# Performance work log

Hardware: AMD Instinct MI355X
Metric: run time of the kernel (lower is better)

The kernel has to match this reference:

```python
import jax, jax.numpy as jnp
import numpy as np

V, D, N, K, T, S = 128000, 128, 4, 4, 16, 5
EPS = 1e-10


def setup_inputs() -> dict:
    key = jax.random.key(0)
    k = jax.random.split(key, 5)
    return {
        "E": jax.random.normal(k[0], (V, D), jnp.float32) * 0.02,
        "bases": jax.random.normal(k[1], (K, N, D, D), jnp.float32) * (1.5 / np.sqrt(D)),
        "tension": jax.random.normal(k[2], (K, N, N), jnp.float32) * 0.1,
        "temperature": jnp.ones((K,), jnp.float32),
        "target_sim": jnp.full((K,), -1.0 / (N - 1), jnp.float32),
        "step_size": jnp.full((K,), 0.1, jnp.float32),
        "gate_logit": jnp.full((K,), -2.0, jnp.float32),
        "decay_base": jnp.asarray(0.8, jnp.float32),
        "sensitivity": jnp.asarray(1.0, jnp.float32),
        "noise": jax.random.normal(k[3], (T, K, S, N, D), jnp.float32),
        "tokens": jax.random.randint(k[4], (T,), 0, V),
    }


def reference(E, bases, tension, temperature, target_sim, step_size, gate_logit,
              decay_base, sensitivity, noise, tokens):
    mask = 1.0 - jnp.eye(N, dtype=E.dtype)
    temp = jnp.clip(jnp.abs(temperature), 0.01, None)
    # gauge interaction weights per foam: softmax over bubbles, self-interaction masked
    interaction = jax.nn.softmax(-tension / temp[:, None, None], axis=-1) * mask  # [K,N,N]
    step = jnp.clip(jnp.abs(step_size), 0.001, 0.5)           # [K]
    gate = jax.nn.sigmoid(gate_logit)                          # [K] noise gate
    sens = jnp.abs(sensitivity)

    def equilibrate(state0, B, inter, tgt, stp, g, nz):
        # state0 [N,D]; B [N,D,D] per-bubble bases; nz [S,N,D] pre-drawn perturbations
        def body(state, eps):
            expr = jnp.einsum('nd,nkd->nk', state, B)          # state_i @ basis_i.T
            expr_n = expr / (jnp.linalg.norm(expr, axis=-1, keepdims=True) + EPS)
            cos = expr_n @ expr_n.T                            # [N,N] pairwise cos-sim
            fmag = (cos - tgt) * inter                         # [N,N] force magnitudes
            diff = expr[:, None, :] - expr[None, :, :]         # [N,N,D]
            diff_n = diff / (jnp.linalg.norm(diff, axis=-1, keepdims=True) + EPS)
            f_shared = (fmag[..., None] * diff_n).sum(axis=1)  # [N,D]
            f_local = jnp.einsum('nk,nkd->nd', f_shared, B)    # back to local gauge
            scale = jnp.linalg.norm(state, axis=-1).mean() + EPS
            return state + stp * f_local + g * eps * scale * 0.01, None
        state, _ = jax.lax.scan(body, state0, nz)
        return state

    def foam_step(x, memory, B, inter, tgt, stp, g, nz):
        # x [D]; memory [N,D]
        mem_mean = memory.mean(axis=0)
        mem_norm = jnp.linalg.norm(mem_mean) + EPS
        x_norm = jnp.linalg.norm(x) + EPS
        nov = 1.0 - (x * mem_mean).sum() / (x_norm * mem_norm)
        novelty = jnp.where(mem_norm > 1e-8, nov, 1.0)
        decay = jax.nn.sigmoid(decay_base - sens * novelty)
        xm = x + decay * mem_mean
        eq = equilibrate(jnp.broadcast_to(xm, (N, D)), B, inter, tgt, stp, g, nz)
        rho = (eq.T @ eq) / ((eq * eq).sum() + EPS)            # trace-normalized density
        mem_new = decay * memory + (1.0 - decay) * eq
        return rho, mem_new

    xs_tok = E[tokens]                                         # [T,D]

    def token_step(memories, inp):
        x, nz_t = inp
        rhos, memories = jax.vmap(foam_step, in_axes=(None, 0, 0, 0, 0, 0, 0, 0))(
            x, memories, bases, interaction, target_sim, step, gate, nz_t)
        rho_mix = rhos.mean(axis=0)                            # [D,D]
        eig = jnp.clip(jnp.linalg.eigvalsh(rho_mix), 1e-12, None)
        eig = eig / eig.sum()
        logits = ((E @ rho_mix) * E).sum(axis=-1)              # born rule [V]
        logp = jax.nn.log_softmax(logits)
        probs = jnp.exp(logp)
        S_rho = -(eig * jnp.clip(jnp.log(eig), -100.0, None)).sum()
        H_tok = -(probs * jnp.clip(logp, -100.0, None)).sum()
        return memories, (probs, S_rho, H_tok, H_tok - S_rho)

    mem0 = jnp.zeros((K, N, D), E.dtype)
    _, (probs, S_rho, H_tok, F_tok) = jax.lax.scan(token_step, mem0, (xs_tok, noise))
    return probs, S_rho, H_tok, F_tok
```

## Files before the change

### kernel.cpp

```cpp
#include <hip/hip_runtime.h>
#include <math.h>

#define V_ 128000
#define D_ 128
#define N_ 4
#define K_ 4
#define T_ 16
#define S_ 5
#define EPSF 1e-10f

#define WS_G      0
#define WS_BEPS   262144
#define WS_BX     917504
#define WS_EQBALL 954368
#define WS_INTER  977408
#define WS_WK     977472
#define WS_SRHO   977728
#define WS_LNZ    977744
#define WS_ZPART  977760
#define WS_HPART  1009760

typedef __attribute__((ext_vector_type(8))) short short8v;
typedef __attribute__((ext_vector_type(4))) float float4v;

__device__ __forceinline__ short bfb(float x) {
    unsigned u = __float_as_uint(x);
    u += 0x7fffu + ((u >> 16) & 1u);
    return (short)(u >> 16);
}

__device__ __forceinline__ void jpair(int x, int r, int& ox, bool& isp) {
    if (x == 15) { ox = r % 15; isp = true; return; }
    int s = x - r; s %= 15; if (s < 0) s += 15;
    if (s == 0) { ox = 15; isp = false; return; }
    int o = 2 * r - x; o %= 15; if (o < 0) o += 15;
    ox = o;
    isp = (s <= 7);
}

__device__ __forceinline__ void rotfast(float app, float aqq, float apq, float& c, float& s) {
    c = 1.f; s = 0.f;
    if (fabsf(apq) > 1e-20f) {
        float tau = (aqq - app) * 0.5f * __builtin_amdgcn_rcpf(apq);
        float sq1 = __builtin_amdgcn_sqrtf(1.f + tau * tau);
        float den = tau + ((tau >= 0.f) ? sq1 : -sq1);
        float tt = __builtin_amdgcn_rcpf(den);
        c = __builtin_amdgcn_rsqf(1.f + tt * tt);
        s = tt * c;
    }
}

__global__ __launch_bounds__(256)
void i2_prep(const float* __restrict__ bases, const float* __restrict__ E,
             const float* __restrict__ noise, const int* __restrict__ tokens,
             const float* __restrict__ tension, const float* __restrict__ temperature,
             float* __restrict__ ws)
{
    int tid = threadIdx.x;
    if (blockIdx.x == 64) {
        if (tid < 4) {
            int k = tid;
            float temp = fmaxf(fabsf(temperature[k]), 0.01f);
            for (int i = 0; i < 4; ++i) {
                float v[4]; float mx = -1e30f;
                for (int j = 0; j < 4; ++j) { v[j] = -tension[k*16 + i*4 + j] / temp; mx = fmaxf(mx, v[j]); }
                float se = 0.f;
                for (int j = 0; j < 4; ++j) { v[j] = expf(v[j] - mx); se += v[j]; }
                for (int j = 0; j < 4; ++j) ws[WS_INTER + k*16 + i*4 + j] = (i == j) ? 0.0f : v[j] / se;
            }
        }
        return;
    }
    int kn = blockIdx.x >> 2, q = blockIdx.x & 3;
    int k = kn >> 2, n = kn & 3;
    __shared__ __align__(16) float Blds[128 * 132];
    const float4* B4 = (const float4*)(bases + (size_t)kn * 16384);
    for (int idx = tid; idx < 4096; idx += 256) {
        int jrow = idx >> 5, c = idx & 31;
        float4 v = B4[jrow * 32 + c];
        *((float4*)&Blds[jrow * 132 + c * 4]) = v;
    }
    __syncthreads();
    int j1 = q * 32 + (tid >> 3);
    int l = tid & 7;
    float accg[16];
#pragma unroll
    for (int i = 0; i < 16; ++i) accg[i] = 0.f;
    for (int c = 0; c < 32; ++c) {
        float4 b1 = *((const float4*)&Blds[j1 * 132 + c * 4]);
#pragma unroll
        for (int i = 0; i < 16; ++i) {
            float4 b2 = *((const float4*)&Blds[(l + 8 * i) * 132 + c * 4]);
            accg[i] += b1.x * b2.x + b1.y * b2.y + b1.z * b2.z + b1.w * b2.w;
        }
    }
#pragma unroll
    for (int i = 0; i < 16; ++i) {
        int j2 = l + 8 * i;
        ws[WS_G + (((size_t)kn * 32 + (j2 >> 2)) * 128 + j1) * 4 + (j2 & 3)] = accg[i];
    }
    __shared__ __align__(16) float vecl[128];
    __shared__ float vred[2][128];
    int jv = tid & 127, ch = tid >> 7;
    for (int vi = q * 24; vi < q * 24 + 24; ++vi) {
        const float* src; int dstoff;
        if (vi < 16) {
            int tt = vi;
            src = E + (size_t)tokens[tt] * 128;
            dstoff = WS_BX + (tt * 4 + k) * 512 + n * 128;
        } else {
            int r2 = vi - 16; int tt = r2 / 5, s2 = r2 % 5;
            size_t off = (size_t)(((tt * 4 + k) * 5 + s2) * 4 + n) * 128;
            src = noise + off;
            dstoff = WS_BEPS + (int)off;
        }
        if (tid < 32) ((float4*)vecl)[tid] = ((const float4*)src)[tid];
        __syncthreads();
        float a2 = 0.f;
        for (int c = ch * 16; c < ch * 16 + 16; ++c) {
            float4 bv = *((const float4*)&Blds[jv * 132 + c * 4]);
            float4 xv = ((const float4*)vecl)[c];
            a2 += bv.x * xv.x + bv.y * xv.y + bv.z * xv.z + bv.w * xv.w;
        }
        vred[ch][jv] = a2;
        __syncthreads();
        if (tid < 128) ws[dstoff + tid] = vred[0][tid] + vred[1][tid];
        __syncthreads();
    }
}

__global__ __launch_bounds__(512, 2)
void kap_all(const float* __restrict__ E, const float* __restrict__ noise,
             const int* __restrict__ tokens, const float* __restrict__ bases,
             const float* __restrict__ target_sim, const float* __restrict__ step_size,
             const float* __restrict__ gate_logit, const float* __restrict__ decay_base,
             const float* __restrict__ sensitivity, float* __restrict__ ws)
{
    const int k = blockIdx.x;
    const int tid = threadIdx.x;
    const int w = tid >> 6;
    const int n = w & 3;
    const int h = w >> 2;
    const int lane = tid & 63;
    const int d0 = lane, d1 = lane + 64;
    const int dG = h * 64 + lane;
    const int kn = k * 4 + n;

    __shared__ float xl[128];
    __shared__ float mlL[128];
    __shared__ __align__(16) float aL[4][128];
    __shared__ float exL[4][128];
    __shared__ float bmmL[4][128];
    __shared__ float interL[16];
    __shared__ float diagP[4], sP[4];
    __shared__ float sq7[4][2];

    float4 gg[32];
    const float4* G4 = (const float4*)(ws + WS_G);
#pragma unroll
    for (int c = 0; c < 32; ++c) gg[c] = G4[((size_t)kn * 32 + c) * 128 + dG];

    if (tid < 16) interL[tid] = ws[WS_INTER + k * 16 + tid];
    if (tid < 128) mlL[tid] = 0.f;
    bmmL[n][dG] = 0.f;

    const float tgt = target_sim[k];
    const float stp = fminf(fmaxf(fabsf(step_size[k]), 0.001f), 0.5f);
    const float gate = 1.0f / (1.0f + expf(-gate_logit[k]));
    const float dbase = decay_base[0];
    const float sens = fabsf(sensitivity[0]);

    float xr = (tid < 128) ? E[(size_t)tokens[0] * 128 + tid] : 0.f;
    __syncthreads();
    float w_inter[4];
#pragma unroll
    for (int m = 0; m < 4; ++m) w_inter[m] = interL[n * 4 + m];

#pragma unroll 1
    for (int t = 0; t < T_; ++t) {
        if (tid < 128) xl[tid] = xr;
        __syncthreads();
        if (t + 1 < T_ && tid < 128) xr = E[(size_t)tokens[t + 1] * 128 + tid];

        float bep0[5], bep1[5], no0[5], no1[5];
#pragma unroll
        for (int s = 0; s < 5; ++s) {
            int nz = (((t * 4 + k) * 5 + s) * 4 + n) * 128;
            bep0[s] = ws[WS_BEPS + nz + d0]; bep1[s] = ws[WS_BEPS + nz + d1];
            no0[s] = noise[nz + d0];         no1[s] = noise[nz + d1];
        }
        float bx0 = ws[WS_BX + (t * 4 + k) * 512 + n * 128 + d0];
        float bx1 = ws[WS_BX + (t * 4 + k) * 512 + n * 128 + d1];

        float x0 = xl[d0], x1 = xl[d1], m0 = mlL[d0], m1 = mlL[d1];
        float vx = x0 * x0 + x1 * x1, vm = m0 * m0 + m1 * m1, vd = x0 * m0 + x1 * m1;
        for (int m = 32; m; m >>= 1) { vx += __shfl_xor(vx, m); vm += __shfl_xor(vm, m); vd += __shfl_xor(vd, m); }
        float xnorm = sqrtf(vx) + EPSF, mnorm = sqrtf(vm) + EPSF;
        float nov = 1.0f - vd / (xnorm * mnorm);
        float novelty = (mnorm > 1e-8f) ? nov : 1.0f;
        const float dec = 1.0f / (1.0f + expf(-(dbase - sens * novelty)));

        float bm0 = bmmL[n][d0], bm1 = bmmL[n][d1];
        float e00 = bx0 + dec * bm0, e01 = bx1 + dec * bm1;
        float u0 = x0 + dec * m0, u1 = x1 + dec * m1;
        float a0 = 0.f, a1 = 0.f, be0 = 0.f, be1 = 0.f;
        exL[n][dG] = (h == 0) ? e00 : e01;
        __syncthreads();

        for (int s = 0; s < 5; ++s) {
            float em0[4], em1[4];
#pragma unroll
            for (int m = 0; m < 4; ++m) { em0[m] = exL[m][d0]; em1[m] = exL[m][d1]; }
            float ex0 = em0[n], ex1 = em1[n];
            float r[5];
#pragma unroll
            for (int m = 0; m < 4; ++m) r[m] = ex0 * em0[m] + ex1 * em1[m];
            float t4 = u0 * u0 + u1 * u1;
            float t5 = (e00 + be0) * a0 + (e01 + be1) * a1;
            float t6 = a0 * (ex0 - e00 - be0) + a1 * (ex1 - e01 - be1);
            r[4] = t4 + 2.f * t5 + t6;
#pragma unroll
            for (int m2 = 32; m2; m2 >>= 1) {
#pragma unroll
                for (int q = 0; q < 5; ++q) r[q] += __shfl_xor(r[q], m2);
            }
            float sn = sqrtf(fmaxf(r[4], 0.f));
            if (lane == 0 && h == 0) { diagP[n] = r[n]; sP[n] = sn; }
            __syncthreads();
            float ssum = ((sP[0] + sP[1]) + sP[2]) + sP[3];
            float cn = gate * (0.25f * ssum + EPSF) * 0.01f;

            float Pnn = r[n];
            float enn = sqrtf(fmaxf(Pnn, 0.f)) + EPSF;
            float fsh0 = 0.f, fsh1 = 0.f;
#pragma unroll
            for (int m = 0; m < 4; ++m) {
                float Pmm = diagP[m];
                float Pnm = r[m];
                float enm = sqrtf(fmaxf(Pmm, 0.f)) + EPSF;
                float cosnm = Pnm / (enn * enm);
                float fm = (cosnm - tgt) * w_inter[m];
                float dnn = sqrtf(fmaxf(Pnn - 2.f * Pnm + Pmm, 0.f)) + EPSF;
                float wq = fm / dnn;
                fsh0 += wq * (ex0 - em0[m]);
                fsh1 += wq * (ex1 - em1[m]);
            }
            a0 += stp * fsh0; a1 += stp * fsh1;
            be0 += cn * bep0[s]; be1 += cn * bep1[s];
            u0 += cn * no0[s];   u1 += cn * no1[s];
            aL[n][d0] = a0; aL[n][d1] = a1;
            const float4* a4 = (const float4*)aL[n];
            float y = 0.f;
#pragma unroll
            for (int c = 0; c < 32; ++c) {
                float4 av = a4[c];
                y += gg[c].x * av.x + gg[c].y * av.y + gg[c].z * av.z + gg[c].w * av.w;
            }
            float exn = ((h == 0) ? e00 : e01) + y + ((h == 0) ? be0 : be1);
            exL[n][dG] = exn;
            __syncthreads();
        }

        {
            const float* Bp = bases + (size_t)kn * 16384;
            float acc = 0.f;
#pragma unroll 8
            for (int j = 0; j < 128; ++j) acc += aL[n][j] * Bp[(size_t)j * 128 + dG];
            float eq = ((h == 0) ? u0 : u1) + acc;
            ws[WS_BEPS + t * 10240 + k * 2560 + n * 128 + dG] = eq;
            unsigned short* eqb = (unsigned short*)(ws + WS_EQBALL);
            {
                int c2 = dG >> 5, lg = (dG >> 3) & 3, j8 = dG & 7;
                eqb[t * 2048 + (c2 * 64 + lg * 16 + kn) * 8 + j8] = (unsigned short)bfb(eq);
            }
            float sq = eq * eq;
            for (int m = 32; m; m >>= 1) sq += __shfl_xor(sq, m);
            if (lane == 0) sq7[n][h] = sq;
            exL[n][dG] = eq;
            __syncthreads();
            if (tid < 4) {
                float s4 = (sq7[0][0] + sq7[0][1]) + (sq7[1][0] + sq7[1][1])
                         + (sq7[2][0] + sq7[2][1]) + (sq7[3][0] + sq7[3][1]);
                ws[WS_WK + t * 16 + 4 * k + tid] = 1.0f / (4.0f * (s4 + EPSF));
            }
            if (n == 0) {
                float eqm = 0.25f * (exL[0][dG] + exL[1][dG] + exL[2][dG] + exL[3][dG]);
                mlL[dG] = dec * mlL[dG] + (1.f - dec) * eqm;
            }
            __syncthreads();
            const float4* Br = (const float4*)(bases + (size_t)kn * 16384 + (size_t)dG * 128);
            const float4* mm4 = (const float4*)mlL;
            float bacc = 0.f;
#pragma unroll 8
            for (int c = 0; c < 32; ++c) {
                float4 mv = mm4[c];
                float4 bv = Br[c];
                bacc += bv.x * mv.x + bv.y * mv.y + bv.z * mv.z + bv.w * mv.w;
            }
            bmmL[n][dG] = bacc;
        }
    }
}

__global__ __launch_bounds__(256, 2)
void mega(const float* __restrict__ E, float* __restrict__ ws, float* __restrict__ out)
{
    int b = blockIdx.x, tid = threadIdx.x;
    if (b < 16) {
        int tt = b;
        __shared__ float Gsh[256];
        __shared__ float Am[16 * 20];
        __shared__ float cR[16], sR[16];
        {
            int i = tid >> 4, j = tid & 15;
            const float4* ra = (const float4*)(ws + WS_BEPS + tt * 10240 + (i >> 2) * 2560 + (i & 3) * 128);
            const float4* rb = (const float4*)(ws + WS_BEPS + tt * 10240 + (j >> 2) * 2560 + (j & 3) * 128);
            float dp = 0.f;
#pragma unroll 8
            for (int c = 0; c < 32; ++c) {
                float4 a = ra[c], b2 = rb[c];
                dp += a.x * b2.x + a.y * b2.y + a.z * b2.z + a.w * b2.w;
            }
            Gsh[tid] = dp;
        }
        __syncthreads();
        if (tid >= 64) return;
        const float* G = Gsh;
        int i0 = tid >> 2, j40 = (tid & 3) * 4;
        float wv4[4];
#pragma unroll
        for (int kk = 0; kk < 4; ++kk) {
            float ss = G[(4*kk+0)*17] + G[(4*kk+1)*17] + G[(4*kk+2)*17] + G[(4*kk+3)*17];
            wv4[kk] = 1.0f / (4.0f * (ss + EPSF));
        }
#pragma unroll
        for (int m = 0; m < 4; ++m) {
            int jjv = j40 + m;
            Am[i0 * 20 + jjv] = sqrtf(wv4[i0 >> 2] * wv4[jjv >> 2]) * G[i0 * 16 + jjv];
        }
        for (int sw = 0; sw < 6; ++sw) {
            for (int r = 0; r < 15; ++r) {
                if (tid < 8) {
                    int p, q;
                    if (tid == 0) { p = 15; q = r % 15; }
                    else { p = (r + tid) % 15; q = (r - tid + 15) % 15; }
                    float c, s;
                    rotfast(Am[p * 20 + p], Am[q * 20 + q], Am[p * 20 + q], c, s);
                    cR[p] = c; sR[p] = -s;
                    cR[q] = c; sR[q] = s;
                }
                int oi; bool ip; jpair(i0, r, oi, ip);
                float ci = cR[i0], siS = sR[i0];
                float nv[4];
#pragma unroll
                for (int m = 0; m < 4; ++m) {
                    int jjv = j40 + m;
                    int oj; bool jp2; jpair(jjv, r, oj, jp2);
                    float cj = cR[jjv], sjS = sR[jjv];
                    float a00 = Am[i0 * 20 + jjv], a01 = Am[i0 * 20 + oj];
                    float a10 = Am[oi * 20 + jjv], a11 = Am[oi * 20 + oj];
                    nv[m] = ci*cj*a00 + ci*sjS*a01 + siS*cj*a10 + siS*sjS*a11;
                }
#pragma unroll
                for (int m = 0; m < 4; ++m) Am[i0 * 20 + j40 + m] = nv[m];
            }
        }
        if (tid == 0) {
            float tot = 112.0f * 1e-12f;
            float lc[16];
            for (int a2 = 0; a2 < 16; ++a2) { lc[a2] = fmaxf(Am[a2 * 20 + a2], 1e-12f); tot += lc[a2]; }
            float S = 0.f;
            for (int a2 = 0; a2 < 16; ++a2) { float pp = lc[a2] / tot; S -= pp * fmaxf(logf(pp), -100.f); }
            float p0 = 1e-12f / tot;
            S -= 112.f * p0 * fmaxf(logf(p0), -100.f);
            out[(size_t)T_ * V_ + tt] = S;
            ws[WS_SRHO + tt] = S;
        }
        return;
    }
    int b2 = b - 16;
    int pass = b2 / 500;
    int bb = b2 - pass * 500;
    int tok0 = pass * 8;
    int lane = tid & 63, wv = tid >> 6;
    const short8v* eqB = (const short8v*)(ws + WS_EQBALL);
    short8v bfr[8][4];
#pragma unroll
    for (int tk = 0; tk < 8; ++tk)
#pragma unroll
        for (int c2 = 0; c2 < 4; ++c2) bfr[tk][c2] = eqB[(tok0 + tk) * 256 + c2 * 64 + lane];
    float wk[8], zl[8];
#pragma unroll
    for (int tk = 0; tk < 8; ++tk) {
        wk[tk] = ws[WS_WK + (tok0 + tk) * 16 + (lane & 15)];
        zl[tk] = 0.f;
    }
    int tilebase = (bb * 4 + wv) * 64;
#pragma unroll
    for (int it = 0; it < 4; ++it) {
        int rowB = tilebase + it * 16;
        const float* Erow = E + (size_t)(rowB + (lane & 15)) * 128 + ((lane >> 4) * 8);
        float4v acc[8];
#pragma unroll
        for (int tk = 0; tk < 8; ++tk) acc[tk] = (float4v){0.f, 0.f, 0.f, 0.f};
#pragma unroll
        for (int c2 = 0; c2 < 4; ++c2) {
            float4 e0 = *((const float4*)(Erow + c2 * 32));
            float4 e1 = *((const float4*)(Erow + c2 * 32 + 4));
            short8v a;
            a[0] = bfb(e0.x); a[1] = bfb(e0.y); a[2] = bfb(e0.z); a[3] = bfb(e0.w);
            a[4] = bfb(e1.x); a[5] = bfb(e1.y); a[6] = bfb(e1.z); a[7] = bfb(e1.w);
#pragma unroll
            for (int tk = 0; tk < 8; ++tk)
                acc[tk] = __builtin_amdgcn_mfma_f32_16x16x32_bf16(a, bfr[tk][c2], acc[tk], 0, 0, 0);
        }
#pragma unroll
        for (int tk = 0; tk < 8; ++tk) {
            float l0 = wk[tk] * acc[tk][0] * acc[tk][0];
            float l1 = wk[tk] * acc[tk][1] * acc[tk][1];
            float l2 = wk[tk] * acc[tk][2] * acc[tk][2];
            float l3 = wk[tk] * acc[tk][3] * acc[tk][3];
#pragma unroll
            for (int m = 1; m <= 8; m <<= 1) {
                l0 += __shfl_xor(l0, m); l1 += __shfl_xor(l1, m);
                l2 += __shfl_xor(l2, m); l3 += __shfl_xor(l3, m);
            }
            if ((lane & 15) == 0) {
                float4 st; st.x = l0; st.y = l1; st.z = l2; st.w = l3;
                *((float4*)(out + (size_t)(tok0 + tk) * V_ + rowB + (lane >> 4) * 4)) = st;
                zl[tk] += __expf(l0) + __expf(l1) + __expf(l2) + __expf(l3);
            }
        }
    }
#pragma unroll
    for (int tk = 0; tk < 8; ++tk) {
        float z = zl[tk];
        z += __shfl_xor(z, 16); z += __shfl_xor(z, 32);
        if (lane == 0) ws[WS_ZPART + (tok0 + tk) * 2000 + bb * 4 + wv] = z;
    }
}

__global__ __launch_bounds__(256)
void zk(float* __restrict__ ws)
{
    int b = blockIdx.x, tid = threadIdx.x;
    double s = 0.0;
    for (int i = tid; i < 2000; i += 256) s += (double)ws[WS_ZPART + b * 2000 + i];
    for (int m = 32; m; m >>= 1) s += __shfl_xor(s, m);
    __shared__ double sr[4];
    if ((tid & 63) == 0) sr[tid >> 6] = s;
    __syncthreads();
    if (tid == 0) ws[WS_LNZ + b] = (float)log(sr[0] + sr[1] + sr[2] + sr[3]);
}

__global__ __launch_bounds__(256)
void fin1(float* __restrict__ ws, float* __restrict__ out)
{
    int b = blockIdx.x, tid = threadIdx.x;
    int tt = b / 125, blk = b - tt * 125;
    int v = blk * 1024 + tid * 4;
    float lnZ = ws[WS_LNZ + tt];
    float* po = out + (size_t)tt * V_ + v;
    float4 l4 = *((const float4*)po);
    float lp0 = l4.x - lnZ, lp1 = l4.y - lnZ, lp2 = l4.z - lnZ, lp3 = l4.w - lnZ;
    float p0 = __expf(lp0), p1 = __expf(lp1), p2 = __expf(lp2), p3 = __expf(lp3);
    float4 st; st.x = p0; st.y = p1; st.z = p2; st.w = p3;
    *((float4*)po) = st;
    float hp = p0 * fmaxf(lp0, -100.f) + p1 * fmaxf(lp1, -100.f)
             + p2 * fmaxf(lp2, -100.f) + p3 * fmaxf(lp3, -100.f);
    for (int m = 32; m; m >>= 1) hp += __shfl_xor(hp, m);
    __shared__ float hr[4];
    if ((tid & 63) == 0) hr[tid >> 6] = hp;
    __syncthreads();
    if (tid == 0) ws[WS_HPART + tt * 125 + blk] = hr[0] + hr[1] + hr[2] + hr[3];
}

__global__ __launch_bounds__(128)
void f2_final(float* __restrict__ ws, float* __restrict__ out)
{
    int t = blockIdx.x, tid = threadIdx.x;
    float s = (tid < 125) ? ws[WS_HPART + t * 125 + tid] : 0.f;
    for (int m = 32; m; m >>= 1) s += __shfl_xor(s, m);
    __shared__ float sr[2];
    if ((tid & 63) == 0) sr[tid >> 6] = s;
    __syncthreads();
    if (tid == 0) {
        float H = -(sr[0] + sr[1]);
        float S = ws[WS_SRHO + t];
        out[(size_t)T_ * V_ + T_ + t] = H;
        out[(size_t)T_ * V_ + 2 * T_ + t] = H - S;
    }
}

extern "C" void kernel_launch(void* const* d_in, const int* in_sizes, int n_in,
                              void* d_out, int out_size, void* d_ws, size_t ws_size,
                              hipStream_t stream)
{
    (void)in_sizes; (void)n_in; (void)out_size; (void)ws_size;
    const float* E           = (const float*)d_in[0];
    const float* bases       = (const float*)d_in[1];
    const float* tension     = (const float*)d_in[2];
    const float* temperature = (const float*)d_in[3];
    const float* target_sim  = (const float*)d_in[4];
    const float* step_size   = (const float*)d_in[5];
    const float* gate_logit  = (const float*)d_in[6];
    const float* decay_base  = (const float*)d_in[7];
    const float* sensitivity = (const float*)d_in[8];
    const float* noise       = (const float*)d_in[9];
    const int*   tokens      = (const int*)d_in[10];
    float* out = (float*)d_out;
    float* ws  = (float*)d_ws;

    i2_prep<<<65, 256, 0, stream>>>(bases, E, noise, tokens, tension, temperature, ws);
    kap_all<<<4, 512, 0, stream>>>(E, noise, tokens, bases, target_sim, step_size,
                                   gate_logit, decay_base, sensitivity, ws);
    mega<<<1016, 256, 0, stream>>>(E, ws, out);
    zk<<<16, 256, 0, stream>>>(ws);
    fin1<<<T_ * 125, 256, 0, stream>>>(ws, out);
    f2_final<<<T_, 128, 0, stream>>>(ws, out);
}
```

Before: 599.8 us.

## Restructure equilibration loop: double-buffer shared state, drop barrier, DPP reductions

Each wave now computes the pairwise dot products and diagonal norms itself from shared expression vectors, using DPP-based wavefront reductions. This removes one of the two block barriers per inner iteration. Expression vectors and the squared-norm partials are double-buffered, and the memory-basis product is kept in registers instead of shared memory. The G matrix is streamed from global memory each iteration rather than held in 128 registers, which lowers register pressure but adds repeated global or cache traffic. Dot products use several independent accumulators to shorten dependency chains.

```diff
diff --git a/kernel.cpp b/kernel.cpp
--- a/kernel.cpp
+++ b/kernel.cpp
@@ -27,6 +27,16 @@
     unsigned u = __float_as_uint(x);
     u += 0x7fffu + ((u >> 16) & 1u);
     return (short)(u >> 16);
+}
+
+__device__ __forceinline__ float wred64(float x) {
+    x += __int_as_float(__builtin_amdgcn_update_dpp(0, __float_as_int(x), 0xB1, 0xf, 0xf, true));
+    x += __int_as_float(__builtin_amdgcn_update_dpp(0, __float_as_int(x), 0x4E, 0xf, 0xf, true));
+    x += __int_as_float(__builtin_amdgcn_update_dpp(0, __float_as_int(x), 0x141, 0xf, 0xf, true));
+    x += __int_as_float(__builtin_amdgcn_update_dpp(0, __float_as_int(x), 0x140, 0xf, 0xf, true));
+    x += __shfl_xor(x, 16);
+    x += __shfl_xor(x, 32);
+    return x;
 }
 
 __device__ __forceinline__ void jpair(int x, int r, int& ox, bool& isp) {
@@ -149,28 +159,26 @@
     __shared__ float xl[128];
     __shared__ float mlL[128];
     __shared__ __align__(16) float aL[4][128];
-    __shared__ float exL[4][128];
-    __shared__ float bmmL[4][128];
+    __shared__ float exb[2][4][128];
     __shared__ float interL[16];
-    __shared__ float diagP[4], sP[4];
+    __shared__ float sPb[2][4][2];
     __shared__ float sq7[4][2];
 
-    float4 gg[32];
-    const float4* G4 = (const float4*)(ws + WS_G);
-#pragma unroll
-    for (int c = 0; c < 32; ++c) gg[c] = G4[((size_t)kn * 32 + c) * 128 + dG];
+    const float4* Gw = (const float4*)(ws + WS_G) + (size_t)kn * 4096 + dG;
+    const float*  Bcol = bases + (size_t)kn * 16384 + dG;
+    const float4* Br0 = (const float4*)(bases + (size_t)kn * 16384 + (size_t)d0 * 128);
+    const float4* Br1 = (const float4*)(bases + (size_t)kn * 16384 + (size_t)d1 * 128);
 
     if (tid < 16) interL[tid] = ws[WS_INTER + k * 16 + tid];
-    if (tid < 128) mlL[tid] = 0.f;
-    bmmL[n][dG] = 0.f;
+    if (tid < 128) { mlL[tid] = 0.f; xl[tid] = E[(size_t)tokens[0] * 128 + tid]; }
 
     const float tgt = target_sim[k];
     const float stp = fminf(fmaxf(fabsf(step_size[k]), 0.001f), 0.5f);
     const float gate = 1.0f / (1.0f + expf(-gate_logit[k]));
     const float dbase = decay_base[0];
     const float sens = fabsf(sensitivity[0]);
-
-    float xr = (tid < 128) ? E[(size_t)tokens[0] * 128 + tid] : 0.f;
+    float bm0 = 0.f, bm1 = 0.f;
+    float xr = 0.f;
     __syncthreads();
     float w_inter[4];
 #pragma unroll
@@ -178,10 +186,6 @@
 
 #pragma unroll 1
     for (int t = 0; t < T_; ++t) {
-        if (tid < 128) xl[tid] = xr;
-        __syncthreads();
-        if (t + 1 < T_ && tid < 128) xr = E[(size_t)tokens[t + 1] * 128 + tid];
-
         float bep0[5], bep1[5], no0[5], no1[5];
 #pragma unroll
         for (int s = 0; s < 5; ++s) {
@@ -191,51 +195,53 @@
         }
         float bx0 = ws[WS_BX + (t * 4 + k) * 512 + n * 128 + d0];
         float bx1 = ws[WS_BX + (t * 4 + k) * 512 + n * 128 + d1];
+        if (t + 1 < T_ && tid < 128) xr = E[(size_t)tokens[t + 1] * 128 + tid];
 
         float x0 = xl[d0], x1 = xl[d1], m0 = mlL[d0], m1 = mlL[d1];
-        float vx = x0 * x0 + x1 * x1, vm = m0 * m0 + m1 * m1, vd = x0 * m0 + x1 * m1;
-        for (int m = 32; m; m >>= 1) { vx += __shfl_xor(vx, m); vm += __shfl_xor(vm, m); vd += __shfl_xor(vd, m); }
+        float vx = wred64(x0 * x0 + x1 * x1);
+        float vm = wred64(m0 * m0 + m1 * m1);
+        float vd = wred64(x0 * m0 + x1 * m1);
         float xnorm = sqrtf(vx) + EPSF, mnorm = sqrtf(vm) + EPSF;
         float nov = 1.0f - vd / (xnorm * mnorm);
         float novelty = (mnorm > 1e-8f) ? nov : 1.0f;
         const float dec = 1.0f / (1.0f + expf(-(dbase - sens * novelty)));
 
-        float bm0 = bmmL[n][d0], bm1 = bmmL[n][d1];
         float e00 = bx0 + dec * bm0, e01 = bx1 + dec * bm1;
         float u0 = x0 + dec * m0, u1 = x1 + dec * m1;
         float a0 = 0.f, a1 = 0.f, be0 = 0.f, be1 = 0.f;
-        exL[n][dG] = (h == 0) ? e00 : e01;
+        {
+            float uh = (h == 0) ? u0 : u1;
+            float r4h = wred64(uh * uh);
+            if (lane == 0) sPb[0][n][h] = r4h;
+        }
+        exb[0][n][dG] = (h == 0) ? e00 : e01;
         __syncthreads();
 
+#pragma unroll
         for (int s = 0; s < 5; ++s) {
+            const int rb = s & 1, wb = rb ^ 1;
             float em0[4], em1[4];
 #pragma unroll
-            for (int m = 0; m < 4; ++m) { em0[m] = exL[m][d0]; em1[m] = exL[m][d1]; }
+            for (int m = 0; m < 4; ++m) { em0[m] = exb[rb][m][d0]; em1[m] = exb[rb][m][d1]; }
             float ex0 = em0[n], ex1 = em1[n];
-            float r[5];
-#pragma unroll
-            for (int m = 0; m < 4; ++m) r[m] = ex0 * em0[m] + ex1 * em1[m];
-            float t4 = u0 * u0 + u1 * u1;
-            float t5 = (e00 + be0) * a0 + (e01 + be1) * a1;
-            float t6 = a0 * (ex0 - e00 - be0) + a1 * (ex1 - e01 - be1);
-            r[4] = t4 + 2.f * t5 + t6;
-#pragma unroll
-            for (int m2 = 32; m2; m2 >>= 1) {
-#pragma unroll
-                for (int q = 0; q < 5; ++q) r[q] += __shfl_xor(r[q], m2);
-            }
-            float sn = sqrtf(fmaxf(r[4], 0.f));
-            if (lane == 0 && h == 0) { diagP[n] = r[n]; sP[n] = sn; }
-            __syncthreads();
-            float ssum = ((sP[0] + sP[1]) + sP[2]) + sP[3];
+            float ssum = sqrtf(fmaxf(sPb[rb][0][0] + sPb[rb][0][1], 0.f))
+                       + sqrtf(fmaxf(sPb[rb][1][0] + sPb[rb][1][1], 0.f))
+                       + sqrtf(fmaxf(sPb[rb][2][0] + sPb[rb][2][1], 0.f))
+                       + sqrtf(fmaxf(sPb[rb][3][0] + sPb[rb][3][1], 0.f));
             float cn = gate * (0.25f * ssum + EPSF) * 0.01f;
 
+            float r[4], dm[4];
+#pragma unroll
+            for (int m = 0; m < 4; ++m) {
+                r[m]  = wred64(ex0 * em0[m] + ex1 * em1[m]);
+                dm[m] = wred64(em0[m] * em0[m] + em1[m] * em1[m]);
+            }
             float Pnn = r[n];
             float enn = sqrtf(fmaxf(Pnn, 0.f)) + EPSF;
             float fsh0 = 0.f, fsh1 = 0.f;
 #pragma unroll
             for (int m = 0; m < 4; ++m) {
-                float Pmm = diagP[m];
+                float Pmm = dm[m];
                 float Pnm = r[m];
                 float enm = sqrtf(fmaxf(Pmm, 0.f)) + EPSF;
                 float cosnm = Pnm / (enn * enm);
@@ -250,33 +256,46 @@
             u0 += cn * no0[s];   u1 += cn * no1[s];
             aL[n][d0] = a0; aL[n][d1] = a1;
             const float4* a4 = (const float4*)aL[n];
-            float y = 0.f;
+            float ya = 0.f, yb = 0.f, yc = 0.f, yd = 0.f;
 #pragma unroll
             for (int c = 0; c < 32; ++c) {
+                float4 gv = Gw[(size_t)c * 128];
                 float4 av = a4[c];
-                y += gg[c].x * av.x + gg[c].y * av.y + gg[c].z * av.z + gg[c].w * av.w;
-            }
+                ya += gv.x * av.x; yb += gv.y * av.y;
+                yc += gv.z * av.z; yd += gv.w * av.w;
+            }
+            float y = (ya + yb) + (yc + yd);
             float exn = ((h == 0) ? e00 : e01) + y + ((h == 0) ? be0 : be1);
-            exL[n][dG] = exn;
+            exb[wb][n][dG] = exn;
+            if (s < 4) {
+                float uh = (h == 0) ? u0 : u1;
+                float ebh = (h == 0) ? (e00 + be0) : (e01 + be1);
+                float ah = (h == 0) ? a0 : a1;
+                float r4h = wred64(uh * uh + 2.f * (ebh * ah) + ah * y);
+                if (lane == 0) sPb[wb][n][h] = r4h;
+            }
             __syncthreads();
         }
 
         {
-            const float* Bp = bases + (size_t)kn * 16384;
-            float acc = 0.f;
-#pragma unroll 8
-            for (int j = 0; j < 128; ++j) acc += aL[n][j] * Bp[(size_t)j * 128 + dG];
-            float eq = ((h == 0) ? u0 : u1) + acc;
+            float eA = 0.f, eB = 0.f, eC = 0.f, eD = 0.f;
+#pragma unroll
+            for (int j = 0; j < 128; j += 4) {
+                eA += aL[n][j]     * Bcol[(size_t)j * 128];
+                eB += aL[n][j + 1] * Bcol[(size_t)(j + 1) * 128];
+                eC += aL[n][j + 2] * Bcol[(size_t)(j + 2) * 128];
+                eD += aL[n][j + 3] * Bcol[(size_t)(j + 3) * 128];
+            }
+            float eq = ((h == 0) ? u0 : u1) + ((eA + eB) + (eC + eD));
             ws[WS_BEPS + t * 10240 + k * 2560 + n * 128 + dG] = eq;
             unsigned short* eqb = (unsigned short*)(ws + WS_EQBALL);
             {
                 int c2 = dG >> 5, lg = (dG >> 3) & 3, j8 = dG & 7;
                 eqb[t * 2048 + (c2 * 64 + lg * 16 + kn) * 8 + j8] = (unsigned short)bfb(eq);
             }
-            float sq = eq * eq;
-            for (int m = 32; m; m >>= 1) sq += __shfl_xor(sq, m);
+            float sq = wred64(eq * eq);
             if (lane == 0) sq7[n][h] = sq;
-            exL[n][dG] = eq;
+            exb[0][n][dG] = eq;
             __syncthreads();
             if (tid < 4) {
                 float s4 = (sq7[0][0] + sq7[0][1]) + (sq7[1][0] + sq7[1][1])
@@ -284,20 +303,23 @@
                 ws[WS_WK + t * 16 + 4 * k + tid] = 1.0f / (4.0f * (s4 + EPSF));
             }
             if (n == 0) {
-                float eqm = 0.25f * (exL[0][dG] + exL[1][dG] + exL[2][dG] + exL[3][dG]);
+                float eqm = 0.25f * (exb[0][0][dG] + exb[0][1][dG] + exb[0][2][dG] + exb[0][3][dG]);
                 mlL[dG] = dec * mlL[dG] + (1.f - dec) * eqm;
             }
+            if (tid < 128) xl[tid] = xr;
             __syncthreads();
-            const float4* Br = (const float4*)(bases + (size_t)kn * 16384 + (size_t)dG * 128);
             const float4* mm4 = (const float4*)mlL;
-            float bacc = 0.f;
-#pragma unroll 8
+            float p0a = 0.f, p0b = 0.f, p0c = 0.f, p0d = 0.f;
+            float p1a = 0.f, p1b = 0.f, p1c = 0.f, p1d = 0.f;
+#pragma unroll
             for (int c = 0; c < 32; ++c) {
                 float4 mv = mm4[c];
-                float4 bv = Br[c];
-                bacc += bv.x * mv.x + bv.y * mv.y + bv.z * mv.z + bv.w * mv.w;
-            }
-            bmmL[n][dG] = bacc;
+                float4 v0 = Br0[c], v1 = Br1[c];
+                p0a += v0.x * mv.x; p0b += v0.y * mv.y; p0c += v0.z * mv.z; p0d += v0.w * mv.w;
+                p1a += v1.x * mv.x; p1b += v1.y * mv.y; p1c += v1.z * mv.z; p1d += v1.w * mv.w;
+            }
+            bm0 = (p0a + p0b) + (p0c + p0d);
+            bm1 = (p1a + p1b) + (p1c + p1d);
         }
     }
 }
@@ -317,7 +339,7 @@
             const float4* rb = (const float4*)(ws + WS_BEPS + tt * 10240 + (j >> 2) * 2560 + (j & 3) * 128);
             float dp = 0.f;
 #pragma unroll 8
-            for (int c = 0; c < 32; ++c) {
+        for (int c = 0; c < 32; ++c) {
                 float4 a = ra[c], b2 = rb[c];
                 dp += a.x * b2.x + a.y * b2.y + a.z * b2.z + a.w * b2.w;
             }
```

Result: slower. 1.013 ms (+68.8%).

## Keep basis rows in AGPRs, stream G per step, use DPP wave reductions

Applied to the files above, without the earlier changes.

Stops holding the 128-float G slice in VGPRs for the whole token loop and instead reads G from global memory on every equilibration step. The per-thread basis row is now preloaded into accumulator registers (AGPRs) via inline asm, so the memory-update matvec no longer reloads it from global memory each token. All 64-lane shuffle reductions are replaced with DPP-based intra-row steps plus two shuffles. The trade is repeated global (likely cached) loads of G inside the hot inner loop in exchange for freeing VGPRs and removing the basis reload.

```diff
diff --git a/kernel.cpp b/kernel.cpp
--- a/kernel.cpp
+++ b/kernel.cpp
@@ -27,6 +27,16 @@
     unsigned u = __float_as_uint(x);
     u += 0x7fffu + ((u >> 16) & 1u);
     return (short)(u >> 16);
+}
+
+__device__ __forceinline__ float wred64(float x) {
+    x += __int_as_float(__builtin_amdgcn_update_dpp(0, __float_as_int(x), 0xB1, 0xf, 0xf, true));
+    x += __int_as_float(__builtin_amdgcn_update_dpp(0, __float_as_int(x), 0x4E, 0xf, 0xf, true));
+    x += __int_as_float(__builtin_amdgcn_update_dpp(0, __float_as_int(x), 0x141, 0xf, 0xf, true));
+    x += __int_as_float(__builtin_amdgcn_update_dpp(0, __float_as_int(x), 0x140, 0xf, 0xf, true));
+    x += __shfl_xor(x, 16);
+    x += __shfl_xor(x, 32);
+    return x;
 }
 
 __device__ __forceinline__ void jpair(int x, int r, int& ox, bool& isp) {
@@ -155,10 +165,19 @@
     __shared__ float diagP[4], sP[4];
     __shared__ float sq7[4][2];
 
-    float4 gg[32];
-    const float4* G4 = (const float4*)(ws + WS_G);
-#pragma unroll
-    for (int c = 0; c < 32; ++c) gg[c] = G4[((size_t)kn * 32 + c) * 128 + dG];
+    float Ab[128];
+    {
+        const float4* Brow = (const float4*)(bases + (size_t)kn * 16384 + (size_t)dG * 128);
+#pragma unroll
+        for (int c = 0; c < 32; ++c) {
+            float4 bv = Brow[c];
+            asm volatile("v_accvgpr_write_b32 %0, %1" : "=a"(Ab[4 * c + 0]) : "v"(bv.x));
+            asm volatile("v_accvgpr_write_b32 %0, %1" : "=a"(Ab[4 * c + 1]) : "v"(bv.y));
+            asm volatile("v_accvgpr_write_b32 %0, %1" : "=a"(Ab[4 * c + 2]) : "v"(bv.z));
+            asm volatile("v_accvgpr_write_b32 %0, %1" : "=a"(Ab[4 * c + 3]) : "v"(bv.w));
+        }
+    }
+    const float4* Gw = (const float4*)(ws + WS_G) + (size_t)kn * 4096 + dG;
 
     if (tid < 16) interL[tid] = ws[WS_INTER + k * 16 + tid];
     if (tid < 128) mlL[tid] = 0.f;
@@ -193,8 +212,9 @@
         float bx1 = ws[WS_BX + (t * 4 + k) * 512 + n * 128 + d1];
 
         float x0 = xl[d0], x1 = xl[d1], m0 = mlL[d0], m1 = mlL[d1];
-        float vx = x0 * x0 + x1 * x1, vm = m0 * m0 + m1 * m1, vd = x0 * m0 + x1 * m1;
-        for (int m = 32; m; m >>= 1) { vx += __shfl_xor(vx, m); vm += __shfl_xor(vm, m); vd += __shfl_xor(vd, m); }
+        float vx = wred64(x0 * x0 + x1 * x1);
+        float vm = wred64(m0 * m0 + m1 * m1);
+        float vd = wred64(x0 * m0 + x1 * m1);
         float xnorm = sqrtf(vx) + EPSF, mnorm = sqrtf(vm) + EPSF;
         float nov = 1.0f - vd / (xnorm * mnorm);
         float novelty = (mnorm > 1e-8f) ? nov : 1.0f;
@@ -220,10 +240,7 @@
             float t6 = a0 * (ex0 - e00 - be0) + a1 * (ex1 - e01 - be1);
             r[4] = t4 + 2.f * t5 + t6;
 #pragma unroll
-            for (int m2 = 32; m2; m2 >>= 1) {
-#pragma unroll
-                for (int q = 0; q < 5; ++q) r[q] += __shfl_xor(r[q], m2);
-            }
+            for (int q = 0; q < 5; ++q) r[q] = wred64(r[q]);
             float sn = sqrtf(fmaxf(r[4], 0.f));
             if (lane == 0 && h == 0) { diagP[n] = r[n]; sP[n] = sn; }
             __syncthreads();
@@ -253,8 +270,9 @@
             float y = 0.f;
 #pragma unroll
             for (int c = 0; c < 32; ++c) {
+                float4 gv = Gw[(size_t)c * 128];
                 float4 av = a4[c];
-                y += gg[c].x * av.x + gg[c].y * av.y + gg[c].z * av.z + gg[c].w * av.w;
+                y += gv.x * av.x + gv.y * av.y + gv.z * av.z + gv.w * av.w;
             }
             float exn = ((h == 0) ? e00 : e01) + y + ((h == 0) ? be0 : be1);
             exL[n][dG] = exn;
@@ -273,8 +291,7 @@
                 int c2 = dG >> 5, lg = (dG >> 3) & 3, j8 = dG & 7;
                 eqb[t * 2048 + (c2 * 64 + lg * 16 + kn) * 8 + j8] = (unsigned short)bfb(eq);
             }
-            float sq = eq * eq;
-            for (int m = 32; m; m >>= 1) sq += __shfl_xor(sq, m);
+            float sq = wred64(eq * eq);
             if (lane == 0) sq7[n][h] = sq;
             exL[n][dG] = eq;
             __syncthreads();
@@ -288,14 +305,17 @@
                 mlL[dG] = dec * mlL[dG] + (1.f - dec) * eqm;
             }
             __syncthreads();
-            const float4* Br = (const float4*)(bases + (size_t)kn * 16384 + (size_t)dG * 128);
             const float4* mm4 = (const float4*)mlL;
             float bacc = 0.f;
-#pragma unroll 8
+#pragma unroll
             for (int c = 0; c < 32; ++c) {
                 float4 mv = mm4[c];
-                float4 bv = Br[c];
-                bacc += bv.x * mv.x + bv.y * mv.y + bv.z * mv.z + bv.w * mv.w;
+                float bxv, byv, bzv, bwv;
+                asm volatile("v_accvgpr_read_b32 %0, %1" : "=v"(bxv) : "a"(Ab[4 * c + 0]));
+                asm volatile("v_accvgpr_read_b32 %0, %1" : "=v"(byv) : "a"(Ab[4 * c + 1]));
+                asm volatile("v_accvgpr_read_b32 %0, %1" : "=v"(bzv) : "a"(Ab[4 * c + 2]));
+                asm volatile("v_accvgpr_read_b32 %0, %1" : "=v"(bwv) : "a"(Ab[4 * c + 3]));
+                bacc += bxv * mv.x + byv * mv.y + bzv * mv.z + bwv * mv.w;
             }
             bmmL[n][dG] = bacc;
         }
```

After: 723.3 us. +20.6%, slower.

## Process all tokens per E tile via LDS-staged eq fragments; stream G from memory

Applied to the files above, without the earlier changes.

The logits kernel now stages all 16 tokens' bf16 equilibrium fragments into shared memory and has each block handle all tokens for its E rows. This halves the number of blocks and reads each E row once instead of twice, removing the duplicated E loads and bf16 conversion. In the sequential kap kernel, the 32 float4 G registers are replaced by per-step global loads, which lowers register pressure but adds memory traffic inside the serial loop. The mega kernel also gains a 64KB shared array in every block, which may limit occupancy.

```diff
diff --git a/kernel.cpp b/kernel.cpp
--- a/kernel.cpp
+++ b/kernel.cpp
@@ -155,10 +155,7 @@
     __shared__ float diagP[4], sP[4];
     __shared__ float sq7[4][2];
 
-    float4 gg[32];
-    const float4* G4 = (const float4*)(ws + WS_G);
-#pragma unroll
-    for (int c = 0; c < 32; ++c) gg[c] = G4[((size_t)kn * 32 + c) * 128 + dG];
+    const float4* Gw = (const float4*)(ws + WS_G) + (size_t)kn * 4096 + dG;
 
     if (tid < 16) interL[tid] = ws[WS_INTER + k * 16 + tid];
     if (tid < 128) mlL[tid] = 0.f;
@@ -253,8 +250,9 @@
             float y = 0.f;
 #pragma unroll
             for (int c = 0; c < 32; ++c) {
+                float4 gv = Gw[(size_t)c * 128];
                 float4 av = a4[c];
-                y += gg[c].x * av.x + gg[c].y * av.y + gg[c].z * av.z + gg[c].w * av.w;
+                y += gv.x * av.x + gv.y * av.y + gv.z * av.z + gv.w * av.w;
             }
             float exn = ((h == 0) ? e00 : e01) + y + ((h == 0) ? be0 : be1);
             exL[n][dG] = exn;
@@ -306,6 +304,7 @@
 void mega(const float* __restrict__ E, float* __restrict__ ws, float* __restrict__ out)
 {
     int b = blockIdx.x, tid = threadIdx.x;
+    __shared__ __align__(16) short8v eqL[4096];
     if (b < 16) {
         int tt = b;
         __shared__ float Gsh[256];
@@ -379,30 +378,27 @@
         return;
     }
     int b2 = b - 16;
-    int pass = b2 / 500;
-    int bb = b2 - pass * 500;
-    int tok0 = pass * 8;
     int lane = tid & 63, wv = tid >> 6;
-    const short8v* eqB = (const short8v*)(ws + WS_EQBALL);
-    short8v bfr[8][4];
-#pragma unroll
-    for (int tk = 0; tk < 8; ++tk)
-#pragma unroll
-        for (int c2 = 0; c2 < 4; ++c2) bfr[tk][c2] = eqB[(tok0 + tk) * 256 + c2 * 64 + lane];
-    float wk[8], zl[8];
-#pragma unroll
-    for (int tk = 0; tk < 8; ++tk) {
-        wk[tk] = ws[WS_WK + (tok0 + tk) * 16 + (lane & 15)];
+    {
+        const float4* src = (const float4*)(ws + WS_EQBALL);
+        float4* dst = (float4*)eqL;
+        for (int i = tid; i < 4096; i += 256) dst[i] = src[i];
+    }
+    float wk[16], zl[16];
+#pragma unroll
+    for (int tk = 0; tk < 16; ++tk) {
+        wk[tk] = ws[WS_WK + tk * 16 + (lane & 15)];
         zl[tk] = 0.f;
     }
-    int tilebase = (bb * 4 + wv) * 64;
-#pragma unroll
+    __syncthreads();
+    int tilebase = (b2 * 4 + wv) * 64;
+#pragma unroll 1
     for (int it = 0; it < 4; ++it) {
         int rowB = tilebase + it * 16;
         const float* Erow = E + (size_t)(rowB + (lane & 15)) * 128 + ((lane >> 4) * 8);
-        float4v acc[8];
-#pragma unroll
-        for (int tk = 0; tk < 8; ++tk) acc[tk] = (float4v){0.f, 0.f, 0.f, 0.f};
+        float4v acc[16];
+#pragma unroll
+        for (int tk = 0; tk < 16; ++tk) acc[tk] = (float4v){0.f, 0.f, 0.f, 0.f};
 #pragma unroll
         for (int c2 = 0; c2 < 4; ++c2) {
             float4 e0 = *((const float4*)(Erow + c2 * 32));
@@ -411,11 +407,11 @@
             a[0] = bfb(e0.x); a[1] = bfb(e0.y); a[2] = bfb(e0.z); a[3] = bfb(e0.w);
             a[4] = bfb(e1.x); a[5] = bfb(e1.y); a[6] = bfb(e1.z); a[7] = bfb(e1.w);
 #pragma unroll
-            for (int tk = 0; tk < 8; ++tk)
-                acc[tk] = __builtin_amdgcn_mfma_f32_16x16x32_bf16(a, bfr[tk][c2], acc[tk], 0, 0, 0);
-        }
-#pragma unroll
-        for (int tk = 0; tk < 8; ++tk) {
+            for (int tk = 0; tk < 16; ++tk)
+                acc[tk] = __builtin_amdgcn_mfma_f32_16x16x32_bf16(a, eqL[tk * 256 + c2 * 64 + lane], acc[tk], 0, 0, 0);
+        }
+#pragma unroll
+        for (int tk = 0; tk < 16; ++tk) {
             float l0 = wk[tk] * acc[tk][0] * acc[tk][0];
             float l1 = wk[tk] * acc[tk][1] * acc[tk][1];
             float l2 = wk[tk] * acc[tk][2] * acc[tk][2];
@@ -427,16 +423,16 @@
             }
             if ((lane & 15) == 0) {
                 float4 st; st.x = l0; st.y = l1; st.z = l2; st.w = l3;
-                *((float4*)(out + (size_t)(tok0 + tk) * V_ + rowB + (lane >> 4) * 4)) = st;
+                *((float4*)(out + (size_t)tk * V_ + rowB + (lane >> 4) * 4)) = st;
                 zl[tk] += __expf(l0) + __expf(l1) + __expf(l2) + __expf(l3);
             }
         }
     }
 #pragma unroll
-    for (int tk = 0; tk < 8; ++tk) {
+    for (int tk = 0; tk < 16; ++tk) {
         float z = zl[tk];
         z += __shfl_xor(z, 16); z += __shfl_xor(z, 32);
-        if (lane == 0) ws[WS_ZPART + (tok0 + tk) * 2000 + bb * 4 + wv] = z;
+        if (lane == 0) ws[WS_ZPART + (size_t)tk * 2000 + b2 * 4 + wv] = z;
     }
 }
 
@@ -514,7 +510,7 @@
     i2_prep<<<65, 256, 0, stream>>>(bases, E, noise, tokens, tension, temperature, ws);
     kap_all<<<4, 512, 0, stream>>>(E, noise, tokens, bases, target_sim, step_size,
                                    gate_logit, decay_base, sensitivity, ws);
-    mega<<<1016, 256, 0, stream>>>(E, ws, out);
+    mega<<<516, 256, 0, stream>>>(E, ws, out);
     zk<<<16, 256, 0, stream>>>(ws);
     fin1<<<T_ * 125, 256, 0, stream>>>(ws, out);
     f2_final<<<T_, 128, 0, stream>>>(ws, out);
```

Result: slower. 898.1 us (+49.7%).
